# Performance work log

Hardware: AMD Instinct MI355X
Metric: run time of the kernel (lower is better)

## Reference

```python
import jax, jax.numpy as jnp
import numpy as np

DIM = 1024
NUM_HEADS = 16
HEAD_DIM = DIM // NUM_HEADS
ROPE_THETA = 10000.0


def rms_norm(x, w):
    # torch nn.RMSNorm with eps=None uses finfo(dtype).eps
    eps = jnp.finfo(x.dtype).eps
    var = jnp.mean(jnp.square(x), axis=-1, keepdims=True)
    return x * jax.lax.rsqrt(var + eps) * w


def rope(x, pos, theta=ROPE_THETA):
    # x: (b, h, n, d), pos: (b, n) float positions. Rotate-half RoPE.
    d = x.shape[-1]
    inv_freq = theta ** (-jnp.arange(0, d, 2, dtype=x.dtype) / d)  # (d/2,)
    ang = pos[:, None, :, None] * inv_freq  # (b, 1, n, d/2)
    cos, sin = jnp.cos(ang), jnp.sin(ang)
    x1, x2 = jnp.split(x, 2, axis=-1)
    return jnp.concatenate([x1 * cos - x2 * sin, x1 * sin + x2 * cos], axis=-1)


def setup_inputs() -> dict:
    key = jax.random.key(0)
    ks = jax.random.split(key, 9)
    b, n = 2, 2048
    s = DIM ** -0.5
    return {
        "tgt": jax.random.normal(ks[0], (b, n, DIM), jnp.float32),
        "src": jax.random.normal(ks[1], (b, n, DIM), jnp.float32),
        "tgt_pos": jax.random.uniform(ks[2], (b, n), jnp.float32) * n,
        "src_pos": jax.random.uniform(ks[3], (b, n), jnp.float32) * n,
        "Wq": jax.random.normal(ks[4], (DIM, DIM), jnp.float32) * s,
        "Wkv": jax.random.normal(ks[5], (DIM, 2 * DIM), jnp.float32) * s,
        "Wo": jax.random.normal(ks[6], (DIM, DIM), jnp.float32) * s,
        "q_norm_w": jnp.ones((HEAD_DIM,), jnp.float32),
        "k_norm_w": jnp.ones((HEAD_DIM,), jnp.float32),
    }


def reference(tgt, src, tgt_pos, src_pos, Wq, Wkv, Wo, q_norm_w, k_norm_w):
    b, n, _ = tgt.shape
    m = src.shape[1]
    h, hd = NUM_HEADS, HEAD_DIM
    # q: (b, h, n, hd)
    q = (tgt @ Wq).reshape(b, n, h, hd).transpose(0, 2, 1, 3)
    # kv layout '(two h d)': split into k and v chunks first
    kv = (src @ Wkv).reshape(b, m, 2, h, hd)
    k = kv[:, :, 0].transpose(0, 2, 1, 3)  # (b, h, m, hd)
    v = kv[:, :, 1].transpose(0, 2, 1, 3)
    q = rms_norm(q, q_norm_w)
    k = rms_norm(k, k_norm_w)
    q = rope(q, tgt_pos)
    k = rope(k, src_pos)
    scores = jnp.einsum("bhnd,bhmd->bhnm", q, k) / (hd ** 0.5)
    attn = jax.nn.softmax(scores, axis=-1)
    x = jnp.einsum("bhnm,bhmd->bhnd", attn, v)
    x = x.transpose(0, 2, 1, 3).reshape(b, n, h * hd)
    return x @ Wo
```

## Files before the change

### kernel.cpp

```cpp
#include <hip/hip_runtime.h>
#include <hip/hip_bf16.h>
#include <stdint.h>

#define DIM 1024
#define NH 16
#define HD 64
#define BATCH 2
#define SEQ 2048
#define ROWS (BATCH*SEQ)
#define NS 2
#define CHUNK (SEQ/NS)
#define NT (CHUNK/64)

typedef __attribute__((ext_vector_type(8))) short bf16x8;
typedef __attribute__((ext_vector_type(4))) float f32x4;
typedef __attribute__((ext_vector_type(16))) float f32x16;
typedef __attribute__((ext_vector_type(4))) unsigned short u16x4;
typedef __attribute__((ext_vector_type(4))) unsigned int u32x4;

static __device__ __forceinline__ unsigned short f2bf(float f) {
    union { float f; uint32_t u; } v; v.f = f;
    uint32_t u = v.u;
    uint32_t rnd = 0x7fffu + ((u >> 16) & 1u);
    return (unsigned short)((u + rnd) >> 16);
}

static __device__ __forceinline__ unsigned cvt_pk_bf16(float lo, float hi) {
    unsigned r;
    asm("v_cvt_pk_bf16_f32 %0, %1, %2" : "=v"(r) : "v"(lo), "v"(hi));
    return r;
}

__global__ void k_conv2(const float* __restrict__ a, const float* __restrict__ b,
                        unsigned short* __restrict__ oa, unsigned short* __restrict__ ob) {
    int blk = blockIdx.x;
    const float* in = (blk < 4096) ? a : b;
    unsigned short* out = (blk < 4096) ? oa : ob;
    int i = ((blk & 4095) * 256 + threadIdx.x) * 4;
    f32x4 v = *(const f32x4*)(in + i);
    u16x4 o;
    o.x = f2bf(v.x); o.y = f2bf(v.y); o.z = f2bf(v.z); o.w = f2bf(v.w);
    *(u16x4*)(out + i) = o;
}

__global__ void k_transpose_all(const float* __restrict__ Wq, const float* __restrict__ Wkv,
                                const float* __restrict__ Wo,
                                unsigned short* __restrict__ WqT, unsigned short* __restrict__ WkvT,
                                unsigned short* __restrict__ WoT) {
    __shared__ float tile[32][33];
    int bx = blockIdx.x;
    const float* W; unsigned short* WT; int N, xb;
    if (bx < 32)      { W = Wq;  WT = WqT;  N = DIM;     xb = bx; }
    else if (bx < 96) { W = Wkv; WT = WkvT; N = 2 * DIM; xb = bx - 32; }
    else              { W = Wo;  WT = WoT;  N = DIM;     xb = bx - 96; }
    const int K = DIM;
    int nt = xb * 32, kt = blockIdx.y * 32;
    int x = threadIdx.x, y = threadIdx.y;
    #pragma unroll
    for (int i = 0; i < 32; i += 8)
        tile[y + i][x] = W[(size_t)(kt + y + i) * N + nt + x];
    __syncthreads();
    #pragma unroll
    for (int i = 0; i < 32; i += 8)
        WT[(size_t)(nt + y + i) * K + kt + x] = f2bf(tile[x][y + i]);
}

__launch_bounds__(256, 3)
__global__ void k_gemm_qkv(const unsigned short* __restrict__ tgt_b,
                           const unsigned short* __restrict__ src_b,
                           const unsigned short* __restrict__ WqT,
                           const unsigned short* __restrict__ WkvT,
                           const float* __restrict__ tpos, const float* __restrict__ spos,
                           const float* __restrict__ qw, const float* __restrict__ kw,
                           unsigned short* __restrict__ q_a, unsigned short* __restrict__ k_f,
                           unsigned short* __restrict__ v_f) {
    __shared__ __align__(16) unsigned short As[128 * 64];
    __shared__ __align__(16) unsigned short Bs[128 * 64];
    const int tid  = threadIdx.x;
    const int wid  = tid >> 6, lane = tid & 63;
    const int l15  = lane & 15, l4 = lane >> 4;
    const int bx = blockIdx.x;
    const unsigned short* A;  const unsigned short* BT;  int n0;
    if (bx < 8) { A = tgt_b; BT = WqT;  n0 = bx * 128; }
    else        { A = src_b; BT = WkvT; n0 = (bx - 8) * 128; }
    const int K = DIM;
    const int m0 = blockIdx.y * 128;
    const int wr = wid >> 1, wc = wid & 1;
    const int srow = lane >> 3, schunk = lane & 7;

    f32x4 acc[4][4] = {};

    for (int kt = 0; kt < K; kt += 64) {
        #pragma unroll
        for (int t = 0; t < 4; ++t) {
            int r  = (t * 4 + wid) * 8 + srow;
            int ck = schunk ^ (r & 7);
            const unsigned short* ga = A  + (size_t)(m0 + r) * K + kt + ck * 8;
            const unsigned short* gb = BT + (size_t)(n0 + r) * K + kt + ck * 8;
            unsigned short* la = As + (t * 4 + wid) * 512 + lane * 8;
            unsigned short* lb = Bs + (t * 4 + wid) * 512 + lane * 8;
            __builtin_amdgcn_global_load_lds((const __attribute__((address_space(1))) void*)ga,
                                             (__attribute__((address_space(3))) void*)la, 16, 0, 0);
            __builtin_amdgcn_global_load_lds((const __attribute__((address_space(1))) void*)gb,
                                             (__attribute__((address_space(3))) void*)lb, 16, 0, 0);
        }
        __syncthreads();
        #pragma unroll
        for (int k0 = 0; k0 < 2; ++k0) {
            bf16x8 af[4], bfr[4];
            int kk = k0 * 32 + l4 * 8;
            #pragma unroll
            for (int i = 0; i < 4; ++i) {
                int ar = wr * 64 + i * 16 + l15;
                af[i]  = *(const bf16x8*)((const char*)As + ar * 128 + ((kk * 2) ^ ((ar & 7) << 4)));
                int br = wc * 64 + i * 16 + l15;
                bfr[i] = *(const bf16x8*)((const char*)Bs + br * 128 + ((kk * 2) ^ ((br & 7) << 4)));
            }
            #pragma unroll
            for (int i = 0; i < 4; ++i)
                #pragma unroll
                for (int j = 0; j < 4; ++j)
                    acc[i][j] = __builtin_amdgcn_mfma_f32_16x16x32_bf16(af[i], bfr[j], acc[i][j], 0, 0, 0);
        }
        __syncthreads();
    }

    const int colbase = n0 + wc * 64;
    const int mode = (bx < 8) ? 0 : ((colbase < 1024) ? 1 : 2);

    if (mode == 2) {
        const int h = (colbase - 1024) >> 6;
        #pragma unroll
        for (int i = 0; i < 4; ++i)
            #pragma unroll
            for (int r = 0; r < 4; ++r) {
                int row = m0 + wr * 64 + i * 16 + l4 * 4 + r;
                int b = row >> 11, mm = row & (SEQ - 1);
                int bh = b * NH + h;
                int t = mm >> 6, ks = (mm >> 5) & 1, kc = (mm >> 4) & 1;
                int hiv = (mm >> 3) & 1, e = mm & 7;
                #pragma unroll
                for (int j = 0; j < 4; ++j) {
                    int dh = j >> 1, l31v = (j & 1) * 16 + l15;
                    size_t idx = (((((size_t)(bh * 32 + t) * 2 + ks) * 2 + kc) * 2 + dh) * 2 + hiv) * 256
                                 + l31v * 8 + e;
                    v_f[idx] = f2bf(acc[i][j][r]);
                }
            }
        return;
    }

    const float* pos = (mode == 0) ? tpos : spos;
    const float* wt  = (mode == 0) ? qw : kw;
    const int h = colbase >> 6;
    const float QS = (mode == 0) ? 0.18033688011112042f : 1.0f;
    const float eps = 1.1920928955078125e-7f;

    float w4[4];
    #pragma unroll
    for (int j = 0; j < 4; ++j) w4[j] = wt[j * 16 + l15];
    float invf0 = __expf(-(float)(2 * l15) * (1.0f / 64.0f) * 9.21034037198f);
    float invf1 = __expf(-(float)(2 * (16 + l15)) * (1.0f / 64.0f) * 9.21034037198f);

    #pragma unroll
    for (int i = 0; i < 4; ++i)
        #pragma unroll
        for (int r = 0; r < 4; ++r) {
            int row = m0 + wr * 64 + i * 16 + l4 * 4 + r;
            float v0 = acc[i][0][r], v1 = acc[i][1][r], v2 = acc[i][2][r], v3 = acc[i][3][r];
            float ssq = v0 * v0 + v1 * v1 + v2 * v2 + v3 * v3;
            ssq += __shfl_xor(ssq, 1, 64);
            ssq += __shfl_xor(ssq, 2, 64);
            ssq += __shfl_xor(ssq, 4, 64);
            ssq += __shfl_xor(ssq, 8, 64);
            float sc = rsqrtf(ssq * (1.0f / 64.0f) + eps);
            v0 *= sc * w4[0]; v1 *= sc * w4[1]; v2 *= sc * w4[2]; v3 *= sc * w4[3];
            float p = pos[row];
            float s0, c0, s1, c1;
            sincosf(p * invf0, &s0, &c0);
            sincosf(p * invf1, &s1, &c1);
            float o0 = (v0 * c0 - v2 * s0) * QS;
            float o1 = (v1 * c1 - v3 * s1) * QS;
            float o2 = (v0 * s0 + v2 * c0) * QS;
            float o3 = (v1 * s1 + v3 * c1) * QS;
            int b = row >> 11, n = row & (SEQ - 1);
            if (mode == 0) {
                unsigned short* dst = q_a + ((size_t)(b * NH + h) * SEQ + n) * 64;
                dst[l15]      = f2bf(o0);
                dst[16 + l15] = f2bf(o1);
                dst[32 + l15] = f2bf(o2);
                dst[48 + l15] = f2bf(o3);
            } else {
                int bh = b * NH + h;
                int t = n >> 6, ksn = (n >> 5) & 1, l31k = n & 31;
                int hik = l15 >> 3, e = l15 & 7;
                size_t base = ((size_t)(bh * 32 + t) * 2 + ksn) * 4;
                k_f[(base + 0) * 512 + hik * 256 + l31k * 8 + e] = f2bf(o0);
                k_f[(base + 1) * 512 + hik * 256 + l31k * 8 + e] = f2bf(o1);
                k_f[(base + 2) * 512 + hik * 256 + l31k * 8 + e] = f2bf(o2);
                k_f[(base + 3) * 512 + hik * 256 + l31k * 8 + e] = f2bf(o3);
            }
        }
}

__launch_bounds__(256)
__global__ void k_gemm_bt(const unsigned short* __restrict__ A,
                          const unsigned short* __restrict__ BT,
                          float* __restrict__ C, int M, int N, int K) {
    __shared__ __align__(16) unsigned short As[128 * 64];
    __shared__ __align__(16) unsigned short Bs[128 * 64];
    const int tid  = threadIdx.x;
    const int wid  = tid >> 6, lane = tid & 63;
    const int l15  = lane & 15, l4 = lane >> 4;
    const int m0 = blockIdx.y * 128, n0 = blockIdx.x * 128;
    const int wr = wid >> 1, wc = wid & 1;
    const int srow = lane >> 3, schunk = lane & 7;

    f32x4 acc[4][4] = {};

    for (int kt = 0; kt < K; kt += 64) {
        #pragma unroll
        for (int t = 0; t < 4; ++t) {
            int r  = (t * 4 + wid) * 8 + srow;
            int ck = schunk ^ (r & 7);
            const unsigned short* ga = A  + (size_t)(m0 + r) * K + kt + ck * 8;
            const unsigned short* gb = BT + (size_t)(n0 + r) * K + kt + ck * 8;
            unsigned short* la = As + (t * 4 + wid) * 512 + lane * 8;
            unsigned short* lb = Bs + (t * 4 + wid) * 512 + lane * 8;
            __builtin_amdgcn_global_load_lds((const __attribute__((address_space(1))) void*)ga,
                                             (__attribute__((address_space(3))) void*)la, 16, 0, 0);
            __builtin_amdgcn_global_load_lds((const __attribute__((address_space(1))) void*)gb,
                                             (__attribute__((address_space(3))) void*)lb, 16, 0, 0);
        }
        __syncthreads();
        #pragma unroll
        for (int k0 = 0; k0 < 2; ++k0) {
            bf16x8 af[4], bfr[4];
            int kk = k0 * 32 + l4 * 8;
            #pragma unroll
            for (int i = 0; i < 4; ++i) {
                int ar = wr * 64 + i * 16 + l15;
                af[i]  = *(const bf16x8*)((const char*)As + ar * 128 + ((kk * 2) ^ ((ar & 7) << 4)));
                int br = wc * 64 + i * 16 + l15;
                bfr[i] = *(const bf16x8*)((const char*)Bs + br * 128 + ((kk * 2) ^ ((br & 7) << 4)));
            }
            #pragma unroll
            for (int i = 0; i < 4; ++i)
                #pragma unroll
                for (int j = 0; j < 4; ++j)
                    acc[i][j] = __builtin_amdgcn_mfma_f32_16x16x32_bf16(af[i], bfr[j], acc[i][j], 0, 0, 0);
        }
        __syncthreads();
    }
    #pragma unroll
    for (int i = 0; i < 4; ++i) {
        int rb = m0 + wr * 64 + i * 16 + l4 * 4;
        #pragma unroll
        for (int j = 0; j < 4; ++j) {
            int col = n0 + wc * 64 + j * 16 + l15;
            #pragma unroll
            for (int r = 0; r < 4; ++r)
                C[(size_t)(rb + r) * N + col] = acc[i][j][r];
        }
    }
}

__launch_bounds__(256, 2)
__global__ void k_attn_part(const unsigned short* __restrict__ q_a,
                            const unsigned short* __restrict__ k_f,
                            const unsigned short* __restrict__ v_f,
                            float* __restrict__ o_part, float* __restrict__ ml) {
    const int tid = threadIdx.x;
    const int wid = tid >> 6, lane = tid & 63;
    const int l31 = lane & 31, hi = lane >> 5;
    const int bh = blockIdx.z, ns = blockIdx.y;
    const int q0 = blockIdx.x * 256 + wid * 64;
    const unsigned short* qb = q_a + (size_t)bh * SEQ * 64;

    bf16x8 qfr[2][4];
    #pragma unroll
    for (int qf = 0; qf < 2; ++qf)
        #pragma unroll
        for (int c = 0; c < 4; ++c)
            qfr[qf][c] = *(const bf16x8*)(qb + (size_t)(q0 + qf * 32 + l31) * 64 + c * 16 + hi * 8);

    const bf16x8* kf8 = (const bf16x8*)k_f;
    const bf16x8* vf8 = (const bf16x8*)v_f;

    f32x16 oacc[2][2] = {};
    float lsum[2] = {0.f, 0.f};

    for (int t = 0; t < NT; ++t) {
        const size_t tg = (size_t)bh * 32 + ns * NT + t;
        const bf16x8* kt = kf8 + tg * 512;
        const bf16x8* vt = vf8 + tg * 512;

        bf16x8 kf[2][4];
        #pragma unroll
        for (int ks = 0; ks < 2; ++ks)
            #pragma unroll
            for (int c = 0; c < 4; ++c)
                kf[ks][c] = kt[((ks * 4 + c) * 2 + hi) * 32 + l31];

        f32x16 sacc[2][2] = {};
        #pragma unroll
        for (int ks = 0; ks < 2; ++ks)
            #pragma unroll
            for (int c = 0; c < 4; ++c) {
                sacc[0][ks] = __builtin_amdgcn_mfma_f32_32x32x16_bf16(kf[ks][c], qfr[0][c], sacc[0][ks], 0, 0, 0);
                sacc[1][ks] = __builtin_amdgcn_mfma_f32_32x32x16_bf16(kf[ks][c], qfr[1][c], sacc[1][ks], 0, 0, 0);
            }

        #pragma unroll
        for (int ks = 0; ks < 2; ++ks)
            #pragma unroll
            for (int kc = 0; kc < 2; ++kc) {
                bf16x8 vf[2];
                #pragma unroll
                for (int dh = 0; dh < 2; ++dh)
                    vf[dh] = vt[(((ks * 2 + kc) * 2 + dh) * 2 + hi) * 32 + l31];
                #pragma unroll
                for (int qf = 0; qf < 2; ++qf) {
                    float p[8];
                    #pragma unroll
                    for (int j = 0; j < 8; ++j)
                        p[j] = __builtin_amdgcn_exp2f(sacc[qf][ks][kc * 8 + j]);
                    lsum[qf] += ((p[0] + p[1]) + (p[2] + p[3])) + ((p[4] + p[5]) + (p[6] + p[7]));
                    unsigned a0 = cvt_pk_bf16(p[0], p[1]);
                    unsigned a1 = cvt_pk_bf16(p[2], p[3]);
                    unsigned b0 = cvt_pk_bf16(p[4], p[5]);
                    unsigned b1 = cvt_pk_bf16(p[6], p[7]);
                    asm("v_permlane32_swap_b32 %0, %1" : "+v"(a0), "+v"(b0));
                    asm("v_permlane32_swap_b32 %0, %1" : "+v"(a1), "+v"(b1));
                    u32x4 w; w.x = a0; w.y = a1; w.z = b0; w.w = b1;
                    bf16x8 pa = __builtin_bit_cast(bf16x8, w);
                    #pragma unroll
                    for (int dh = 0; dh < 2; ++dh)
                        oacc[qf][dh] = __builtin_amdgcn_mfma_f32_32x32x16_bf16(pa, vf[dh], oacc[qf][dh], 0, 0, 0);
                }
            }
    }

    lsum[0] += __shfl_xor(lsum[0], 32, 64);
    lsum[1] += __shfl_xor(lsum[1], 32, 64);

    const size_t chunkbase = ((size_t)bh * NS + ns) * SEQ;
    #pragma unroll
    for (int qf = 0; qf < 2; ++qf) {
        #pragma unroll
        for (int r = 0; r < 16; ++r) {
            int qrow = (r & 3) + 8 * (r >> 2) + 4 * hi;
            size_t rowbase = (chunkbase + q0 + qf * 32 + qrow) * 64;
            o_part[rowbase + l31]      = oacc[qf][0][r];
            o_part[rowbase + 32 + l31] = oacc[qf][1][r];
        }
        if (hi == 0)
            ml[chunkbase + q0 + qf * 32 + l31] = lsum[qf];
    }
}

__launch_bounds__(256)
__global__ void k_combine(const float* __restrict__ o_part, const float* __restrict__ ml,
                          unsigned short* __restrict__ xo) {
    int wid = threadIdx.x >> 6, lane = threadIdx.x & 63;
    int idx = blockIdx.x * 4 + wid;
    int bh = idx >> 11, q = idx & (SEQ - 1);
    const size_t base = ((size_t)bh * NS) * SEQ + q;

    float O = 0.f, L = 0.f;
    #pragma unroll
    for (int i = 0; i < NS; ++i) {
        L += ml[base + (size_t)i * SEQ];
        O += o_part[(base + (size_t)i * SEQ) * 64 + lane];
    }
    int b = bh >> 4, h = bh & 15;
    xo[(size_t)(b * SEQ + q) * DIM + h * 64 + lane] = f2bf(O / L);
}

extern "C" void kernel_launch(void* const* d_in, const int* in_sizes, int n_in,
                              void* d_out, int out_size, void* d_ws, size_t ws_size,
                              hipStream_t stream) {
    const float* tgt  = (const float*)d_in[0];
    const float* src  = (const float*)d_in[1];
    const float* tpos = (const float*)d_in[2];
    const float* spos = (const float*)d_in[3];
    const float* Wq   = (const float*)d_in[4];
    const float* Wkv  = (const float*)d_in[5];
    const float* Wo   = (const float*)d_in[6];
    const float* qw   = (const float*)d_in[7];
    const float* kw   = (const float*)d_in[8];
    float* out = (float*)d_out;
    char* ws = (char*)d_ws;

    unsigned short* tgt_b = (unsigned short*)(ws);
    unsigned short* src_b = (unsigned short*)(ws + ( 8u << 20));
    unsigned short* WqT   = (unsigned short*)(ws + (16u << 20));
    unsigned short* WkvT  = (unsigned short*)(ws + (18u << 20));
    unsigned short* WoT   = (unsigned short*)(ws + (22u << 20));
    float*          o_prt = (float*)         (ws + (48u << 20));
    unsigned short* q_a   = (unsigned short*)(ws + (88u << 20));
    unsigned short* k_f   = (unsigned short*)(ws + (96u << 20));
    unsigned short* v_f   = (unsigned short*)(ws + (104u << 20));
    float*          ml    = (float*)         (ws + (112u << 20));
    unsigned short* x_b   = (unsigned short*)(ws);

    k_conv2<<<8192, 256, 0, stream>>>(tgt, src, tgt_b, src_b);
    k_transpose_all<<<dim3(128, 32), dim3(32, 8), 0, stream>>>(Wq, Wkv, Wo, WqT, WkvT, WoT);
    k_gemm_qkv<<<dim3(24, 32), 256, 0, stream>>>(tgt_b, src_b, WqT, WkvT,
                                                 tpos, spos, qw, kw, q_a, k_f, v_f);
    k_attn_part<<<dim3(SEQ / 256, NS, BATCH * NH), 256, 0, stream>>>(q_a, k_f, v_f, o_prt, ml);
    k_combine<<<BATCH * NH * SEQ / 4, 256, 0, stream>>>(o_prt, ml, x_b);
    k_gemm_bt<<<dim3( 8, 32), 256, 0, stream>>>(x_b, WoT, out, ROWS, DIM, DIM);
}
```

Measured before the change: 128.4 us.

## Merge conversion and transpose kernels; halve attention query tile per wave

The separate bf16 conversion and weight-transpose kernels become one launch, saving a kernel launch and its gap. The attention kernel now has each wave handle 32 query rows instead of 64, which doubles the grid and raises the occupancy hint to 4 blocks per CU. The aim is better latency hiding and CU utilisation. The cost is that each K/V tile is loaded twice as often per query, so global and L2 traffic for K and V doubles.

```diff
diff --git a/kernel.cpp b/kernel.cpp
--- a/kernel.cpp
+++ b/kernel.cpp
@@ -31,31 +31,33 @@
     return r;
 }
 
-__global__ void k_conv2(const float* __restrict__ a, const float* __restrict__ b,
-                        unsigned short* __restrict__ oa, unsigned short* __restrict__ ob) {
+__global__ void k_pre(const float* __restrict__ tgt, const float* __restrict__ src,
+                      unsigned short* __restrict__ tgt_b, unsigned short* __restrict__ src_b,
+                      const float* __restrict__ Wq, const float* __restrict__ Wkv,
+                      const float* __restrict__ Wo,
+                      unsigned short* __restrict__ WqT, unsigned short* __restrict__ WkvT,
+                      unsigned short* __restrict__ WoT) {
+    __shared__ float tile[32][33];
     int blk = blockIdx.x;
-    const float* in = (blk < 4096) ? a : b;
-    unsigned short* out = (blk < 4096) ? oa : ob;
-    int i = ((blk & 4095) * 256 + threadIdx.x) * 4;
-    f32x4 v = *(const f32x4*)(in + i);
-    u16x4 o;
-    o.x = f2bf(v.x); o.y = f2bf(v.y); o.z = f2bf(v.z); o.w = f2bf(v.w);
-    *(u16x4*)(out + i) = o;
-}
-
-__global__ void k_transpose_all(const float* __restrict__ Wq, const float* __restrict__ Wkv,
-                                const float* __restrict__ Wo,
-                                unsigned short* __restrict__ WqT, unsigned short* __restrict__ WkvT,
-                                unsigned short* __restrict__ WoT) {
-    __shared__ float tile[32][33];
-    int bx = blockIdx.x;
+    if (blk < 8192) {
+        const float* in = (blk < 4096) ? tgt : src;
+        unsigned short* out = (blk < 4096) ? tgt_b : src_b;
+        int i = ((blk & 4095) * 256 + threadIdx.x) * 4;
+        f32x4 v = *(const f32x4*)(in + i);
+        u16x4 o;
+        o.x = f2bf(v.x); o.y = f2bf(v.y); o.z = f2bf(v.z); o.w = f2bf(v.w);
+        *(u16x4*)(out + i) = o;
+        return;
+    }
+    int bp = blk - 8192;
+    int bx = bp & 127, by = bp >> 7;
     const float* W; unsigned short* WT; int N, xb;
     if (bx < 32)      { W = Wq;  WT = WqT;  N = DIM;     xb = bx; }
     else if (bx < 96) { W = Wkv; WT = WkvT; N = 2 * DIM; xb = bx - 32; }
     else              { W = Wo;  WT = WoT;  N = DIM;     xb = bx - 96; }
     const int K = DIM;
-    int nt = xb * 32, kt = blockIdx.y * 32;
-    int x = threadIdx.x, y = threadIdx.y;
+    int nt = xb * 32, kt = by * 32;
+    int x = threadIdx.x & 31, y = threadIdx.x >> 5;
     #pragma unroll
     for (int i = 0; i < 32; i += 8)
         tile[y + i][x] = W[(size_t)(kt + y + i) * N + nt + x];
@@ -265,7 +267,7 @@
     }
 }
 
-__launch_bounds__(256, 2)
+__launch_bounds__(256, 4)
 __global__ void k_attn_part(const unsigned short* __restrict__ q_a,
                             const unsigned short* __restrict__ k_f,
                             const unsigned short* __restrict__ v_f,
@@ -274,41 +276,32 @@
     const int wid = tid >> 6, lane = tid & 63;
     const int l31 = lane & 31, hi = lane >> 5;
     const int bh = blockIdx.z, ns = blockIdx.y;
-    const int q0 = blockIdx.x * 256 + wid * 64;
+    const int q0 = blockIdx.x * 128 + wid * 32;
     const unsigned short* qb = q_a + (size_t)bh * SEQ * 64;
 
-    bf16x8 qfr[2][4];
-    #pragma unroll
-    for (int qf = 0; qf < 2; ++qf)
-        #pragma unroll
-        for (int c = 0; c < 4; ++c)
-            qfr[qf][c] = *(const bf16x8*)(qb + (size_t)(q0 + qf * 32 + l31) * 64 + c * 16 + hi * 8);
+    bf16x8 qfr[4];
+    #pragma unroll
+    for (int c = 0; c < 4; ++c)
+        qfr[c] = *(const bf16x8*)(qb + (size_t)(q0 + l31) * 64 + c * 16 + hi * 8);
 
     const bf16x8* kf8 = (const bf16x8*)k_f;
     const bf16x8* vf8 = (const bf16x8*)v_f;
 
-    f32x16 oacc[2][2] = {};
-    float lsum[2] = {0.f, 0.f};
+    f32x16 oacc[2] = {};
+    float lsum = 0.f;
 
     for (int t = 0; t < NT; ++t) {
         const size_t tg = (size_t)bh * 32 + ns * NT + t;
         const bf16x8* kt = kf8 + tg * 512;
         const bf16x8* vt = vf8 + tg * 512;
 
-        bf16x8 kf[2][4];
+        f32x16 sacc[2] = {};
         #pragma unroll
         for (int ks = 0; ks < 2; ++ks)
             #pragma unroll
-            for (int c = 0; c < 4; ++c)
-                kf[ks][c] = kt[((ks * 4 + c) * 2 + hi) * 32 + l31];
-
-        f32x16 sacc[2][2] = {};
-        #pragma unroll
-        for (int ks = 0; ks < 2; ++ks)
-            #pragma unroll
             for (int c = 0; c < 4; ++c) {
-                sacc[0][ks] = __builtin_amdgcn_mfma_f32_32x32x16_bf16(kf[ks][c], qfr[0][c], sacc[0][ks], 0, 0, 0);
-                sacc[1][ks] = __builtin_amdgcn_mfma_f32_32x32x16_bf16(kf[ks][c], qfr[1][c], sacc[1][ks], 0, 0, 0);
+                bf16x8 kf = kt[((ks * 4 + c) * 2 + hi) * 32 + l31];
+                sacc[ks] = __builtin_amdgcn_mfma_f32_32x32x16_bf16(kf, qfr[c], sacc[ks], 0, 0, 0);
             }
 
         #pragma unroll
@@ -319,44 +312,37 @@
                 #pragma unroll
                 for (int dh = 0; dh < 2; ++dh)
                     vf[dh] = vt[(((ks * 2 + kc) * 2 + dh) * 2 + hi) * 32 + l31];
-                #pragma unroll
-                for (int qf = 0; qf < 2; ++qf) {
-                    float p[8];
-                    #pragma unroll
-                    for (int j = 0; j < 8; ++j)
-                        p[j] = __builtin_amdgcn_exp2f(sacc[qf][ks][kc * 8 + j]);
-                    lsum[qf] += ((p[0] + p[1]) + (p[2] + p[3])) + ((p[4] + p[5]) + (p[6] + p[7]));
-                    unsigned a0 = cvt_pk_bf16(p[0], p[1]);
-                    unsigned a1 = cvt_pk_bf16(p[2], p[3]);
-                    unsigned b0 = cvt_pk_bf16(p[4], p[5]);
-                    unsigned b1 = cvt_pk_bf16(p[6], p[7]);
-                    asm("v_permlane32_swap_b32 %0, %1" : "+v"(a0), "+v"(b0));
-                    asm("v_permlane32_swap_b32 %0, %1" : "+v"(a1), "+v"(b1));
-                    u32x4 w; w.x = a0; w.y = a1; w.z = b0; w.w = b1;
-                    bf16x8 pa = __builtin_bit_cast(bf16x8, w);
-                    #pragma unroll
-                    for (int dh = 0; dh < 2; ++dh)
-                        oacc[qf][dh] = __builtin_amdgcn_mfma_f32_32x32x16_bf16(pa, vf[dh], oacc[qf][dh], 0, 0, 0);
-                }
-            }
-    }
-
-    lsum[0] += __shfl_xor(lsum[0], 32, 64);
-    lsum[1] += __shfl_xor(lsum[1], 32, 64);
+                float p[8];
+                #pragma unroll
+                for (int j = 0; j < 8; ++j)
+                    p[j] = __builtin_amdgcn_exp2f(sacc[ks][kc * 8 + j]);
+                lsum += ((p[0] + p[1]) + (p[2] + p[3])) + ((p[4] + p[5]) + (p[6] + p[7]));
+                unsigned a0 = cvt_pk_bf16(p[0], p[1]);
+                unsigned a1 = cvt_pk_bf16(p[2], p[3]);
+                unsigned b0 = cvt_pk_bf16(p[4], p[5]);
+                unsigned b1 = cvt_pk_bf16(p[6], p[7]);
+                asm("v_permlane32_swap_b32 %0, %1" : "+v"(a0), "+v"(b0));
+                asm("v_permlane32_swap_b32 %0, %1" : "+v"(a1), "+v"(b1));
+                u32x4 w; w.x = a0; w.y = a1; w.z = b0; w.w = b1;
+                bf16x8 pa = __builtin_bit_cast(bf16x8, w);
+                #pragma unroll
+                for (int dh = 0; dh < 2; ++dh)
+                    oacc[dh] = __builtin_amdgcn_mfma_f32_32x32x16_bf16(pa, vf[dh], oacc[dh], 0, 0, 0);
+            }
+    }
+
+    lsum += __shfl_xor(lsum, 32, 64);
 
     const size_t chunkbase = ((size_t)bh * NS + ns) * SEQ;
     #pragma unroll
-    for (int qf = 0; qf < 2; ++qf) {
-        #pragma unroll
-        for (int r = 0; r < 16; ++r) {
-            int qrow = (r & 3) + 8 * (r >> 2) + 4 * hi;
-            size_t rowbase = (chunkbase + q0 + qf * 32 + qrow) * 64;
-            o_part[rowbase + l31]      = oacc[qf][0][r];
-            o_part[rowbase + 32 + l31] = oacc[qf][1][r];
-        }
-        if (hi == 0)
-            ml[chunkbase + q0 + qf * 32 + l31] = lsum[qf];
-    }
+    for (int r = 0; r < 16; ++r) {
+        int qrow = (r & 3) + 8 * (r >> 2) + 4 * hi;
+        size_t rowbase = (chunkbase + q0 + qrow) * 64;
+        o_part[rowbase + l31]      = oacc[0][r];
+        o_part[rowbase + 32 + l31] = oacc[1][r];
+    }
+    if (hi == 0)
+        ml[chunkbase + q0 + l31] = lsum;
 }
 
 __launch_bounds__(256)
@@ -404,11 +390,10 @@
     float*          ml    = (float*)         (ws + (112u << 20));
     unsigned short* x_b   = (unsigned short*)(ws);
 
-    k_conv2<<<8192, 256, 0, stream>>>(tgt, src, tgt_b, src_b);
-    k_transpose_all<<<dim3(128, 32), dim3(32, 8), 0, stream>>>(Wq, Wkv, Wo, WqT, WkvT, WoT);
+    k_pre<<<12288, 256, 0, stream>>>(tgt, src, tgt_b, src_b, Wq, Wkv, Wo, WqT, WkvT, WoT);
     k_gemm_qkv<<<dim3(24, 32), 256, 0, stream>>>(tgt_b, src_b, WqT, WkvT,
                                                  tpos, spos, qw, kw, q_a, k_f, v_f);
-    k_attn_part<<<dim3(SEQ / 256, NS, BATCH * NH), 256, 0, stream>>>(q_a, k_f, v_f, o_prt, ml);
+    k_attn_part<<<dim3(SEQ / 128, NS, BATCH * NH), 256, 0, stream>>>(q_a, k_f, v_f, o_prt, ml);
     k_combine<<<BATCH * NH * SEQ / 4, 256, 0, stream>>>(o_prt, ml, x_b);
     k_gemm_bt<<<dim3( 8, 32), 256, 0, stream>>>(x_b, WoT, out, ROWS, DIM, DIM);
 }
```

After: 132.9 us. +3.5%, slower.
